# Optimization experiments

Measured on AMD Instinct MI355X. Metric: run time of the kernel, lower is better.

## Reference

```python
import jax, jax.numpy as jnp
import numpy as np

N_NODES = 100000
N_EDGES = 3200000
IN_CH, HID, OUT_CH = 11, 64, 1


def setup_inputs() -> dict:
    key = jax.random.key(0)
    ks = jax.random.split(key, 10)
    x = jax.random.normal(ks[0], (N_NODES, IN_CH), dtype=jnp.float32)
    edge_index = jax.random.randint(ks[1], (2, N_EDGES), 0, N_NODES, dtype=jnp.int64)
    s = lambda k, shape, fan_in: jax.random.normal(k, shape, jnp.float32) * (1.0 / np.sqrt(fan_in))
    return {
        "x": x,
        "edge_index": edge_index,
        # conv1: lin_l acts on aggregated neighbors (has bias), lin_r on root (no bias)
        "Wl1": s(ks[2], (HID, IN_CH), IN_CH), "bl1": jnp.zeros((HID,), jnp.float32),
        "Wr1": s(ks[3], (HID, IN_CH), IN_CH),
        "Wl2": s(ks[4], (HID, HID), HID), "bl2": jnp.zeros((HID,), jnp.float32),
        "Wr2": s(ks[5], (HID, HID), HID),
        "Wlin": s(ks[6], (OUT_CH, HID), HID), "blin": jnp.zeros((OUT_CH,), jnp.float32),
    }


def _sage_conv(x, src, dst, Wl, bl, Wr):
    # mean aggregation of source features onto destination nodes
    msg = x[src]                                            # [E, d] gather
    agg = jax.ops.segment_sum(msg, dst, num_segments=N_NODES)          # [N, d]
    cnt = jax.ops.segment_sum(jnp.ones_like(dst, jnp.float32), dst, num_segments=N_NODES)
    mean = agg / jnp.maximum(cnt, 1.0)[:, None]             # isolated nodes -> 0
    return mean @ Wl.T + bl + x @ Wr.T


def reference(x, edge_index, Wl1, bl1, Wr1, Wl2, bl2, Wr2, Wlin, blin):
    src, dst = edge_index[0], edge_index[1]
    h = jax.nn.relu(_sage_conv(x, src, dst, Wl1, bl1, Wr1))
    h = jax.nn.relu(_sage_conv(h, src, dst, Wl2, bl2, Wr2))
    return h @ Wlin.T + blin
```

## Files before the change

kernel.cpp:

```cpp
#include <hip/hip_runtime.h>
#include <hip/hip_fp16.h>

#define IN_CH 11
#define HID 64
#define PAD 64
#define OVCAP 16384
#define NBLK 256
#define BSH 7

typedef _Float16 half8_t __attribute__((ext_vector_type(8)));
typedef float f32x4_t __attribute__((ext_vector_type(4)));

__device__ __forceinline__ int xcd_gid(int blk) {
    return ((blk & 7) << 5) | (blk >> 3);
}

__global__ void k_prep(const float* __restrict__ x, const float* __restrict__ Wl2,
                       const float* __restrict__ Wr2, unsigned* __restrict__ xphu,
                       __half* __restrict__ wl2h, __half* __restrict__ wr2h,
                       int* __restrict__ ovcnt, int N) {
    int i = blockIdx.x * blockDim.x + threadIdx.x;
    if (i == 0) *ovcnt = 0;
    if (i < HID * HID) {
        wl2h[i] = __float2half_rn(Wl2[i]);
        wr2h[i] = __float2half_rn(Wr2[i]);
    }
    if (i < (N + 1) * 8) {
        int n = i >> 3, j = (i & 7) * 2;
        float a = 0.f, b = 0.f;
        if (n < N) {
            if (j < IN_CH) a = x[n * IN_CH + j];
            if (j + 1 < IN_CH) b = x[n * IN_CH + j + 1];
        }
        unsigned lo = (unsigned)__half_as_ushort(__float2half_rn(a));
        unsigned hi = (unsigned)__half_as_ushort(__float2half_rn(b));
        xphu[i] = lo | (hi << 16);
    }
}


__global__ __launch_bounds__(256) void k_hist(const int* __restrict__ dst,
        int* __restrict__ hist, int E, int csz, int nbkt) {
    __shared__ int h[800];
    int tid = threadIdx.x, blk = blockIdx.x;
    int gid = xcd_gid(blk);
    for (int t = tid; t < nbkt; t += 256) h[t] = 0;
    __syncthreads();
    int c0 = blk * csz, c1 = min(c0 + csz, E);
    for (int base = c0; base < c1; base += 1024) {
        int d[4]; bool ok[4];
        #pragma unroll
        for (int k = 0; k < 4; k++) {
            int e = base + tid + k * 256;
            ok[k] = e < c1;
            d[k] = ok[k] ? __builtin_nontemporal_load(&dst[e]) : 0;
        }
        #pragma unroll
        for (int k = 0; k < 4; k++)
            if (ok[k]) atomicAdd(&h[d[k] >> BSH], 1);
    }
    __syncthreads();
    for (int t = tid; t < nbkt; t += 256) hist[t * NBLK + gid] = h[t];
}

__global__ __launch_bounds__(256) void k_scanA(int* __restrict__ hist,
        int* __restrict__ btot) {
    __shared__ int wsum[4];
    int b = blockIdx.x, tid = threadIdx.x;
    int lane = tid & 63, wv = tid >> 6;
    int v = hist[b * NBLK + tid];
    int inc = v;
    #pragma unroll
    for (int off = 1; off < 64; off <<= 1) {
        int t = __shfl_up(inc, off);
        if (lane >= off) inc += t;
    }
    if (lane == 63) wsum[wv] = inc;
    __syncthreads();
    int base = 0;
    #pragma unroll
    for (int w = 0; w < 4; w++) base += (w < wv) ? wsum[w] : 0;
    hist[b * NBLK + tid] = base + inc - v;
    if (tid == 255) btot[b] = base + inc;
}

__global__ __launch_bounds__(1024) void k_scanB(const int* __restrict__ btot,
        int* __restrict__ bstart, int nbkt) {
    __shared__ int wsum[16];
    int tid = threadIdx.x;
    int lane = tid & 63, wv = tid >> 6;
    int v = (tid < nbkt) ? btot[tid] : 0;
    int inc = v;
    #pragma unroll
    for (int off = 1; off < 64; off <<= 1) {
        int t = __shfl_up(inc, off);
        if (lane >= off) inc += t;
    }
    if (lane == 63) wsum[wv] = inc;
    __syncthreads();
    int base = 0;
    #pragma unroll
    for (int w = 0; w < 16; w++) base += (w < wv) ? wsum[w] : 0;
    if (tid < nbkt) bstart[tid] = base + inc - v;
}

__global__ __launch_bounds__(256) void k_scatter(const int* __restrict__ src,
        const int* __restrict__ dst, const int* __restrict__ hist,
        const int* __restrict__ bstart,
        unsigned* __restrict__ ebuf, int E, int csz, int nbkt) {
    __shared__ int cur[800];
    int tid = threadIdx.x, blk = blockIdx.x;
    int gid = xcd_gid(blk);
    for (int t = tid; t < nbkt; t += 256)
        cur[t] = hist[t * NBLK + gid] + bstart[t];
    __syncthreads();
    int c0 = blk * csz, c1 = min(c0 + csz, E);
    for (int base = c0; base < c1; base += 1024) {
        int d[4], s[4], slot[4];
        bool ok[4];
        #pragma unroll
        for (int k = 0; k < 4; k++) {
            int e = base + tid + k * 256;
            ok[k] = e < c1;
            d[k] = ok[k] ? __builtin_nontemporal_load(&dst[e]) : 0;
            s[k] = ok[k] ? __builtin_nontemporal_load(&src[e]) : 0;
        }
        #pragma unroll
        for (int k = 0; k < 4; k++)
            if (ok[k]) slot[k] = atomicAdd(&cur[d[k] >> BSH], 1);
        #pragma unroll
        for (int k = 0; k < 4; k++)
            if (ok[k]) ebuf[slot[k]] = ((unsigned)s[k] << 7) | (unsigned)(d[k] & 127);
    }
}

__global__ __launch_bounds__(256) void k_bbuild(const unsigned* __restrict__ ebuf,
        const int* __restrict__ bstart, const int* __restrict__ btot,
        int* __restrict__ cnt, int* __restrict__ col64,
        int* __restrict__ ovcnt, int* __restrict__ ov, int N) {
    __shared__ int lc[128];
    __shared__ int colsh[128 * PAD];
    int tid = threadIdx.x, b = blockIdx.x;
    int lo = b << BSH, hi = min(lo + 128, N);
    #pragma unroll
    for (int i = 0; i < 8; i++)
        ((int4*)colsh)[tid + i * 256] = make_int4(N, N, N, N);
    if (tid < 128) lc[tid] = 0;
    __syncthreads();
    int cs = bstart[b], cc = btot[b];
    for (int i = tid; i < cc; i += 256) {
        unsigned p = __builtin_nontemporal_load(&ebuf[cs + i]);
        int row = (int)(p & 127u);
        int sv  = (int)(p >> 7);
        int r = atomicAdd(&lc[row], 1);
        if (r < PAD) {
            colsh[(row << 6) | r] = sv;
        } else {
            int q = atomicAdd(ovcnt, 1);
            if (q < OVCAP) { ov[2 * q] = lo + row; ov[2 * q + 1] = sv; }
        }
    }
    __syncthreads();
    int nn = hi - lo;
    int4* dst4 = (int4*)col64 + (size_t)lo * 16;
    for (int i = tid; i < nn * 16; i += 256) dst4[i] = ((int4*)colsh)[i];
    if (tid < nn) cnt[lo + tid] = lc[tid];
}

__global__ void k_agg1(const unsigned* __restrict__ xphu,
                       const int* __restrict__ col64,
                       float* __restrict__ agg1, int N) {
    int lane = threadIdx.x & 63;
    int n = blockIdx.x * 4 + (threadIdx.x >> 6);
    if (n >= N) return;
    int c8 = lane & 7, sub = lane >> 3;
    const int* cb = col64 + n * PAD;
    int s[8];
    #pragma unroll
    for (int jj = 0; jj < 8; jj++) s[jj] = __builtin_nontemporal_load(&cb[sub + 8 * jj]);
    unsigned v[8];
    #pragma unroll
    for (int jj = 0; jj < 8; jj++) v[jj] = xphu[s[jj] * 8 + c8];
    __half2 a2 = __floats2half2_rn(0.f, 0.f);
    #pragma unroll
    for (int jj = 0; jj < 8; jj++) a2 = __hadd2(a2, *(__half2*)&v[jj]);
    float2 f = __half22float2(a2);
    #pragma unroll
    for (int off = 8; off <= 32; off <<= 1) {
        f.x += __shfl_xor(f.x, off);
        f.y += __shfl_xor(f.y, off);
    }
    if (lane < 8) ((float2*)agg1)[n * 8 + lane] = f;
}

__global__ void k_ov1(const int* __restrict__ ovcnt, const int* __restrict__ ov,
                      const float* __restrict__ x, float* __restrict__ agg1) {
    int c = *ovcnt; if (c > OVCAP) c = OVCAP;
    for (int i = blockIdx.x * blockDim.x + threadIdx.x; i < c;
         i += gridDim.x * blockDim.x) {
        int d = ov[2 * i], s = ov[2 * i + 1];
        for (int ch = 0; ch < IN_CH; ch++)
            atomicAdd(&agg1[d * 16 + ch], x[s * IN_CH + ch]);
    }
}

__global__ void k_dense1(const float* __restrict__ x, const float* __restrict__ agg1,
                         const int* __restrict__ cnt, const float* __restrict__ Wl,
                         const float* __restrict__ bl, const float* __restrict__ Wr,
                         unsigned* __restrict__ h1h, int N) {
    int lane = threadIdx.x & 63;
    int n = blockIdx.x * 4 + (threadIdx.x >> 6);
    if (n > N) return;
    if (n == N) {
        if (lane < 32) h1h[n * 32 + lane] = 0u;
        return;
    }
    int deg = cnt[n];
    float inv = deg > 0 ? 1.f / (float)deg : 0.f;
    float mv = (lane < 16) ? agg1[n * 16 + lane] * inv : 0.f;
    float xv = (lane < IN_CH) ? x[n * IN_CH + lane] : 0.f;
    float h = bl[lane];
    #pragma unroll
    for (int c = 0; c < IN_CH; c++)
        h += Wl[lane * IN_CH + c] * __shfl(mv, c) + Wr[lane * IN_CH + c] * __shfl(xv, c);
    h = fmaxf(h, 0.f);
    unsigned my = (unsigned)__half_as_ushort(__float2half_rn(h));
    unsigned nx = __shfl_down(my, 1);
    if ((lane & 1) == 0) h1h[n * 32 + (lane >> 1)] = my | (nx << 16);
}

__global__ void k_agg2(const uint4* __restrict__ h1h4, const int* __restrict__ col64,
                       float* __restrict__ agg2, int N) {
    int lane = threadIdx.x & 63;
    int n = blockIdx.x * 4 + (threadIdx.x >> 6);
    if (n >= N) return;
    int c8 = lane & 7, sub = lane >> 3;
    const int* cb = col64 + n * PAD;
    int s[8];
    #pragma unroll
    for (int jj = 0; jj < 8; jj++) s[jj] = __builtin_nontemporal_load(&cb[sub + 8 * jj]);
    uint4 v[8];
    #pragma unroll
    for (int jj = 0; jj < 8; jj++) v[jj] = h1h4[s[jj] * 8 + c8];
    __half2 a2[4];
    #pragma unroll
    for (int t = 0; t < 4; t++) a2[t] = __floats2half2_rn(0.f, 0.f);
    #pragma unroll
    for (int jj = 0; jj < 8; jj++) {
        a2[0] = __hadd2(a2[0], *(__half2*)&v[jj].x);
        a2[1] = __hadd2(a2[1], *(__half2*)&v[jj].y);
        a2[2] = __hadd2(a2[2], *(__half2*)&v[jj].z);
        a2[3] = __hadd2(a2[3], *(__half2*)&v[jj].w);
    }
    float acc[8];
    #pragma unroll
    for (int t = 0; t < 4; t++) {
        float2 f = __half22float2(a2[t]);
        acc[2 * t] = f.x; acc[2 * t + 1] = f.y;
    }
    #pragma unroll
    for (int off = 8; off <= 32; off <<= 1) {
        #pragma unroll
        for (int t = 0; t < 8; t++) acc[t] += __shfl_xor(acc[t], off);
    }
    float val = acc[0];
    #pragma unroll
    for (int t = 1; t < 8; t++) if (sub == t) val = acc[t];
    agg2[n * 64 + 8 * c8 + sub] = val;
}

__global__ void k_ov2(const int* __restrict__ ovcnt, const int* __restrict__ ov,
                      const unsigned* __restrict__ h1h, float* __restrict__ agg2) {
    int c = *ovcnt; if (c > OVCAP) c = OVCAP;
    const __half* h1 = (const __half*)h1h;
    for (int i = blockIdx.x * blockDim.x + threadIdx.x; i < c;
         i += gridDim.x * blockDim.x) {
        int d = ov[2 * i], s = ov[2 * i + 1];
        for (int ch = 0; ch < HID; ch++)
            atomicAdd(&agg2[d * 64 + ch], __half2float(h1[s * 64 + ch]));
    }
}

__global__ __launch_bounds__(256) void k_dense2(
    const float4* __restrict__ agg2_4, const int* __restrict__ cnt,
    const uint4* __restrict__ h1h_u4,
    const __half* __restrict__ wl2h, const __half* __restrict__ wr2h,
    const float* __restrict__ bl, const float* __restrict__ Wlin,
    const float* __restrict__ blin, float* __restrict__ out, int N) {
    union U { uint4 u; half8_t h; };
    int lane = threadIdx.x & 63;
    int wave = blockIdx.x * 4 + (threadIdx.x >> 6);
    int nwaves = gridDim.x * 4;
    int r16 = lane & 15, quad = lane >> 4;
    const uint4* wlu = (const uint4*)wl2h;
    const uint4* wru = (const uint4*)wr2h;
    half8_t bfr[4][4];
    #pragma unroll
    for (int tt = 0; tt < 4; tt++) {
        int o = tt * 16 + r16;
        U t0, t1, t2, t3;
        t0.u = wlu[o * 8 + quad];
        t1.u = wlu[o * 8 + 4 + quad];
        t2.u = wru[o * 8 + quad];
        t3.u = wru[o * 8 + 4 + quad];
        bfr[tt][0] = t0.h; bfr[tt][1] = t1.h; bfr[tt][2] = t2.h; bfr[tt][3] = t3.h;
    }
    float bl_c[4], wl_c[4];
    #pragma unroll
    for (int tt = 0; tt < 4; tt++) {
        bl_c[tt] = bl[tt * 16 + r16];
        wl_c[tt] = Wlin[tt * 16 + r16];
    }
    float b0 = blin[0];
    int ntiles = (N + 15) >> 4;
    for (int t = wave; t < ntiles; t += nwaves) {
        int nb = t * 16;
        int n = nb + r16; if (n >= N) n = N - 1;
        int deg = cnt[n];
        float inv = deg > 0 ? 1.f / (float)deg : 0.f;
        float4 m0 = agg2_4[n * 16 + quad * 2];
        float4 m1 = agg2_4[n * 16 + quad * 2 + 1];
        float4 m2 = agg2_4[n * 16 + 8 + quad * 2];
        float4 m3 = agg2_4[n * 16 + 8 + quad * 2 + 1];
        half8_t a0h, a1h;
        a0h[0] = (_Float16)(m0.x * inv); a0h[1] = (_Float16)(m0.y * inv);
        a0h[2] = (_Float16)(m0.z * inv); a0h[3] = (_Float16)(m0.w * inv);
        a0h[4] = (_Float16)(m1.x * inv); a0h[5] = (_Float16)(m1.y * inv);
        a0h[6] = (_Float16)(m1.z * inv); a0h[7] = (_Float16)(m1.w * inv);
        a1h[0] = (_Float16)(m2.x * inv); a1h[1] = (_Float16)(m2.y * inv);
        a1h[2] = (_Float16)(m2.z * inv); a1h[3] = (_Float16)(m2.w * inv);
        a1h[4] = (_Float16)(m3.x * inv); a1h[5] = (_Float16)(m3.y * inv);
        a1h[6] = (_Float16)(m3.z * inv); a1h[7] = (_Float16)(m3.w * inv);
        U a2, a3;
        a2.u = h1h_u4[n * 8 + quad];
        a3.u = h1h_u4[n * 8 + 4 + quad];
        float p0 = 0.f, p1 = 0.f, p2 = 0.f, p3 = 0.f;
        #pragma unroll
        for (int tt = 0; tt < 4; tt++) {
            f32x4_t c = {0.f, 0.f, 0.f, 0.f};
            c = __builtin_amdgcn_mfma_f32_16x16x32_f16(a0h, bfr[tt][0], c, 0, 0, 0);
            c = __builtin_amdgcn_mfma_f32_16x16x32_f16(a1h, bfr[tt][1], c, 0, 0, 0);
            c = __builtin_amdgcn_mfma_f32_16x16x32_f16(a2.h, bfr[tt][2], c, 0, 0, 0);
            c = __builtin_amdgcn_mfma_f32_16x16x32_f16(a3.h, bfr[tt][3], c, 0, 0, 0);
            p0 += fmaxf(c[0] + bl_c[tt], 0.f) * wl_c[tt];
            p1 += fmaxf(c[1] + bl_c[tt], 0.f) * wl_c[tt];
            p2 += fmaxf(c[2] + bl_c[tt], 0.f) * wl_c[tt];
            p3 += fmaxf(c[3] + bl_c[tt], 0.f) * wl_c[tt];
        }
        #pragma unroll
        for (int off = 1; off <= 8; off <<= 1) {
            p0 += __shfl_xor(p0, off); p1 += __shfl_xor(p1, off);
            p2 += __shfl_xor(p2, off); p3 += __shfl_xor(p3, off);
        }
        if (r16 == 0) {
            int nn = nb + quad * 4;
            if (nn + 3 < N) {
                ((float4*)out)[nn >> 2] = make_float4(p0 + b0, p1 + b0, p2 + b0, p3 + b0);
            } else {
                if (nn + 0 < N) out[nn + 0] = p0 + b0;
                if (nn + 1 < N) out[nn + 1] = p1 + b0;
                if (nn + 2 < N) out[nn + 2] = p2 + b0;
                if (nn + 3 < N) out[nn + 3] = p3 + b0;
            }
        }
    }
}


extern "C" void kernel_launch(void* const* d_in, const int* in_sizes, int n_in,
                              void* d_out, int out_size, void* d_ws, size_t ws_size,
                              hipStream_t stream) {
    const float* x    = (const float*)d_in[0];
    const int*   ei   = (const int*)d_in[1];
    const float* Wl1  = (const float*)d_in[2];
    const float* bl1  = (const float*)d_in[3];
    const float* Wr1  = (const float*)d_in[4];
    const float* Wl2  = (const float*)d_in[5];
    const float* bl2  = (const float*)d_in[6];
    const float* Wr2  = (const float*)d_in[7];
    const float* Wlin = (const float*)d_in[8];
    const float* blin = (const float*)d_in[9];
    float* out = (float*)d_out;

    int N = in_sizes[0] / IN_CH;
    int E = in_sizes[1] / 2;
    const int* srcp = ei;
    const int* dstp = ei + E;

    int* ws       = (int*)d_ws;
    int* cnt      = ws;
    int* ovcnt    = ws + N;
    int* col64    = ws + 100032;
    int* hist     = ws + 100032;
    unsigned* xph = (unsigned*)(ws + 6500032);
    unsigned* ebuf= (unsigned*)(ws + 7300064);
    float* agg1   = (float*)(ws + 7300064);
    float* agg2   = (float*)(ws + 6500032);
    unsigned* h1h = (unsigned*)(ws + 12900096);
    int* ov       = ws + 16100128;
    __half* wl2h  = (__half*)(ws + 16132896);
    __half* wr2h  = (__half*)(ws + 16134944);
    int* btot     = ws + 16136992;
    int* bstart   = ws + 16138016;

    int nbkt = (N + 127) >> BSH;
    int csz  = (E + NBLK - 1) / NBLK;

    k_prep   <<<((N + 1) * 8 + 255) / 256, 256, 0, stream>>>(x, Wl2, Wr2, xph,
                                                             wl2h, wr2h, ovcnt, N);
    k_hist   <<<NBLK, 256, 0, stream>>>(dstp, hist, E, csz, nbkt);
    k_scanA  <<<nbkt, 256, 0, stream>>>(hist, btot);
    k_scanB  <<<1, 1024, 0, stream>>>(btot, bstart, nbkt);
    k_scatter<<<NBLK, 256, 0, stream>>>(srcp, dstp, hist, bstart, ebuf, E, csz, nbkt);
    k_bbuild <<<nbkt, 256, 0, stream>>>(ebuf, bstart, btot, cnt, col64,
                                        ovcnt, ov, N);

    k_agg1   <<<(N + 3) / 4, 256, 0, stream>>>(xph, col64, agg1, N);
    k_ov1    <<<8, 256, 0, stream>>>(ovcnt, ov, x, agg1);
    k_dense1 <<<(N + 4) / 4, 256, 0, stream>>>(x, agg1, cnt, Wl1, bl1, Wr1, h1h, N);

    k_agg2   <<<(N + 3) / 4, 256, 0, stream>>>((const uint4*)h1h, col64, agg2, N);
    k_ov2    <<<8, 256, 0, stream>>>(ovcnt, ov, h1h, agg2);

    k_dense2 <<<512, 256, 0, stream>>>((const float4*)agg2, cnt, (const uint4*)h1h,
                                       wl2h, wr2h, bl2, Wlin, blin, out, N);
}
```

Before: 294.6 us.

## Replace histogram+scan+scatter with fixed-capacity per-XCD bucket slots via global atomics

Merges the histogram, two-level scan and scatter kernels into one build kernel. Each block counts its bucket histogram locally, then reserves space in fixed-capacity per-(XCD, bucket) cells with one global atomicAdd per bucket. Edges that overflow a cell go to the overflow list. This removes three kernel launches and the global prefix scan, and the block count doubles. In exchange the per-bucket counts are hardcoded for this graph size, and edge ordering within a bucket is no longer deterministic.

```diff
diff --git a/kernel.cpp b/kernel.cpp
--- a/kernel.cpp
+++ b/kernel.cpp
@@ -5,22 +5,21 @@
 #define HID 64
 #define PAD 64
 #define OVCAP 16384
-#define NBLK 256
+#define NBLK 512
 #define BSH 7
+#define NBKT 782
+#define CAP8 768
 
 typedef _Float16 half8_t __attribute__((ext_vector_type(8)));
 typedef float f32x4_t __attribute__((ext_vector_type(4)));
-
-__device__ __forceinline__ int xcd_gid(int blk) {
-    return ((blk & 7) << 5) | (blk >> 3);
-}
 
 __global__ void k_prep(const float* __restrict__ x, const float* __restrict__ Wl2,
                        const float* __restrict__ Wr2, unsigned* __restrict__ xphu,
                        __half* __restrict__ wl2h, __half* __restrict__ wr2h,
-                       int* __restrict__ ovcnt, int N) {
+                       int* __restrict__ ovcnt, int* __restrict__ bcnt8, int N) {
     int i = blockIdx.x * blockDim.x + threadIdx.x;
     if (i == 0) *ovcnt = 0;
+    if (i < 8 * NBKT) bcnt8[i] = 0;
     if (i < HID * HID) {
         wl2h[i] = __float2half_rn(Wl2[i]);
         wr2h[i] = __float2half_rn(Wr2[i]);
@@ -38,13 +37,16 @@
     }
 }
 
-
-__global__ __launch_bounds__(256) void k_hist(const int* __restrict__ dst,
-        int* __restrict__ hist, int E, int csz, int nbkt) {
-    __shared__ int h[800];
+__global__ __launch_bounds__(256) void k_build(const int* __restrict__ src,
+        const int* __restrict__ dst, unsigned* __restrict__ ebuf,
+        int* __restrict__ bcnt8, int* __restrict__ ovcnt, int* __restrict__ ov,
+        int E, int csz) {
+    __shared__ int h[NBKT];
+    __shared__ int cur[NBKT];
+    __shared__ int lim[NBKT];
     int tid = threadIdx.x, blk = blockIdx.x;
-    int gid = xcd_gid(blk);
-    for (int t = tid; t < nbkt; t += 256) h[t] = 0;
+    int xcd = blk & 7;
+    for (int t = tid; t < NBKT; t += 256) h[t] = 0;
     __syncthreads();
     int c0 = blk * csz, c1 = min(c0 + csz, E);
     for (int base = c0; base < c1; base += 1024) {
@@ -53,68 +55,22 @@
         for (int k = 0; k < 4; k++) {
             int e = base + tid + k * 256;
             ok[k] = e < c1;
-            d[k] = ok[k] ? __builtin_nontemporal_load(&dst[e]) : 0;
+            d[k] = ok[k] ? dst[e] : 0;
         }
         #pragma unroll
         for (int k = 0; k < 4; k++)
             if (ok[k]) atomicAdd(&h[d[k] >> BSH], 1);
     }
     __syncthreads();
-    for (int t = tid; t < nbkt; t += 256) hist[t * NBLK + gid] = h[t];
-}
-
-__global__ __launch_bounds__(256) void k_scanA(int* __restrict__ hist,
-        int* __restrict__ btot) {
-    __shared__ int wsum[4];
-    int b = blockIdx.x, tid = threadIdx.x;
-    int lane = tid & 63, wv = tid >> 6;
-    int v = hist[b * NBLK + tid];
-    int inc = v;
-    #pragma unroll
-    for (int off = 1; off < 64; off <<= 1) {
-        int t = __shfl_up(inc, off);
-        if (lane >= off) inc += t;
-    }
-    if (lane == 63) wsum[wv] = inc;
-    __syncthreads();
-    int base = 0;
-    #pragma unroll
-    for (int w = 0; w < 4; w++) base += (w < wv) ? wsum[w] : 0;
-    hist[b * NBLK + tid] = base + inc - v;
-    if (tid == 255) btot[b] = base + inc;
-}
-
-__global__ __launch_bounds__(1024) void k_scanB(const int* __restrict__ btot,
-        int* __restrict__ bstart, int nbkt) {
-    __shared__ int wsum[16];
-    int tid = threadIdx.x;
-    int lane = tid & 63, wv = tid >> 6;
-    int v = (tid < nbkt) ? btot[tid] : 0;
-    int inc = v;
-    #pragma unroll
-    for (int off = 1; off < 64; off <<= 1) {
-        int t = __shfl_up(inc, off);
-        if (lane >= off) inc += t;
-    }
-    if (lane == 63) wsum[wv] = inc;
-    __syncthreads();
-    int base = 0;
-    #pragma unroll
-    for (int w = 0; w < 16; w++) base += (w < wv) ? wsum[w] : 0;
-    if (tid < nbkt) bstart[tid] = base + inc - v;
-}
-
-__global__ __launch_bounds__(256) void k_scatter(const int* __restrict__ src,
-        const int* __restrict__ dst, const int* __restrict__ hist,
-        const int* __restrict__ bstart,
-        unsigned* __restrict__ ebuf, int E, int csz, int nbkt) {
-    __shared__ int cur[800];
-    int tid = threadIdx.x, blk = blockIdx.x;
-    int gid = xcd_gid(blk);
-    for (int t = tid; t < nbkt; t += 256)
-        cur[t] = hist[t * NBLK + gid] + bstart[t];
-    __syncthreads();
-    int c0 = blk * csz, c1 = min(c0 + csz, E);
+    for (int t = tid; t < NBKT; t += 256) {
+        int hc = h[t];
+        int cell = xcd * NBKT + t;
+        int base = cell * CAP8;
+        int off = (hc > 0) ? atomicAdd(&bcnt8[cell], hc) : 0;
+        cur[t] = base + off;
+        lim[t] = base + CAP8;
+    }
+    __syncthreads();
     for (int base = c0; base < c1; base += 1024) {
         int d[4], s[4], slot[4];
         bool ok[4];
@@ -122,20 +78,27 @@
         for (int k = 0; k < 4; k++) {
             int e = base + tid + k * 256;
             ok[k] = e < c1;
-            d[k] = ok[k] ? __builtin_nontemporal_load(&dst[e]) : 0;
+            d[k] = ok[k] ? dst[e] : 0;
             s[k] = ok[k] ? __builtin_nontemporal_load(&src[e]) : 0;
         }
         #pragma unroll
         for (int k = 0; k < 4; k++)
             if (ok[k]) slot[k] = atomicAdd(&cur[d[k] >> BSH], 1);
         #pragma unroll
-        for (int k = 0; k < 4; k++)
-            if (ok[k]) ebuf[slot[k]] = ((unsigned)s[k] << 7) | (unsigned)(d[k] & 127);
+        for (int k = 0; k < 4; k++) {
+            if (!ok[k]) continue;
+            if (slot[k] < lim[d[k] >> BSH]) {
+                ebuf[slot[k]] = ((unsigned)s[k] << 7) | (unsigned)(d[k] & 127);
+            } else {
+                int q = atomicAdd(ovcnt, 1);
+                if (q < OVCAP) { ov[2 * q] = d[k]; ov[2 * q + 1] = s[k]; }
+            }
+        }
     }
 }
 
 __global__ __launch_bounds__(256) void k_bbuild(const unsigned* __restrict__ ebuf,
-        const int* __restrict__ bstart, const int* __restrict__ btot,
+        const int* __restrict__ bcnt8,
         int* __restrict__ cnt, int* __restrict__ col64,
         int* __restrict__ ovcnt, int* __restrict__ ov, int N) {
     __shared__ int lc[128];
@@ -147,17 +110,21 @@
         ((int4*)colsh)[tid + i * 256] = make_int4(N, N, N, N);
     if (tid < 128) lc[tid] = 0;
     __syncthreads();
-    int cs = bstart[b], cc = btot[b];
-    for (int i = tid; i < cc; i += 256) {
-        unsigned p = __builtin_nontemporal_load(&ebuf[cs + i]);
-        int row = (int)(p & 127u);
-        int sv  = (int)(p >> 7);
-        int r = atomicAdd(&lc[row], 1);
-        if (r < PAD) {
-            colsh[(row << 6) | r] = sv;
-        } else {
-            int q = atomicAdd(ovcnt, 1);
-            if (q < OVCAP) { ov[2 * q] = lo + row; ov[2 * q + 1] = sv; }
+    for (int x = 0; x < 8; x++) {
+        int cell = x * NBKT + b;
+        int cc = min(bcnt8[cell], CAP8);
+        const unsigned* seg = ebuf + (size_t)cell * CAP8;
+        for (int i = tid; i < cc; i += 256) {
+            unsigned p = __builtin_nontemporal_load(&seg[i]);
+            int row = (int)(p & 127u);
+            int sv  = (int)(p >> 7);
+            int r = atomicAdd(&lc[row], 1);
+            if (r < PAD) {
+                colsh[(row << 6) | r] = sv;
+            } else {
+                int q = atomicAdd(ovcnt, 1);
+                if (q < OVCAP) { ov[2 * q] = lo + row; ov[2 * q + 1] = sv; }
+            }
         }
     }
     __syncthreads();
@@ -391,29 +358,23 @@
     int* cnt      = ws;
     int* ovcnt    = ws + N;
     int* col64    = ws + 100032;
-    int* hist     = ws + 100032;
     unsigned* xph = (unsigned*)(ws + 6500032);
     unsigned* ebuf= (unsigned*)(ws + 7300064);
+    int* bcnt8    = ws + 12104672;
     float* agg1   = (float*)(ws + 7300064);
     float* agg2   = (float*)(ws + 6500032);
     unsigned* h1h = (unsigned*)(ws + 12900096);
     int* ov       = ws + 16100128;
     __half* wl2h  = (__half*)(ws + 16132896);
     __half* wr2h  = (__half*)(ws + 16134944);
-    int* btot     = ws + 16136992;
-    int* bstart   = ws + 16138016;
-
-    int nbkt = (N + 127) >> BSH;
-    int csz  = (E + NBLK - 1) / NBLK;
+
+    int csz = (E + NBLK - 1) / NBLK;
 
     k_prep   <<<((N + 1) * 8 + 255) / 256, 256, 0, stream>>>(x, Wl2, Wr2, xph,
-                                                             wl2h, wr2h, ovcnt, N);
-    k_hist   <<<NBLK, 256, 0, stream>>>(dstp, hist, E, csz, nbkt);
-    k_scanA  <<<nbkt, 256, 0, stream>>>(hist, btot);
-    k_scanB  <<<1, 1024, 0, stream>>>(btot, bstart, nbkt);
-    k_scatter<<<NBLK, 256, 0, stream>>>(srcp, dstp, hist, bstart, ebuf, E, csz, nbkt);
-    k_bbuild <<<nbkt, 256, 0, stream>>>(ebuf, bstart, btot, cnt, col64,
-                                        ovcnt, ov, N);
+                                                             wl2h, wr2h, ovcnt,
+                                                             bcnt8, N);
+    k_build  <<<NBLK, 256, 0, stream>>>(srcp, dstp, ebuf, bcnt8, ovcnt, ov, E, csz);
+    k_bbuild <<<NBKT, 256, 0, stream>>>(ebuf, bcnt8, cnt, col64, ovcnt, ov, N);
 
     k_agg1   <<<(N + 3) / 4, 256, 0, stream>>>(xph, col64, agg1, N);
     k_ov1    <<<8, 256, 0, stream>>>(ovcnt, ov, x, agg1);
```

After: 263.2 us. 10.6% less time.
